# Performance work log

Measured on AMD Instinct MI355X. Metric: run time of the kernel, lower is better.

## Reference

```python
import jax, jax.numpy as jnp
import numpy as np

B, T, C = 4, 4096, 1024
HEAD = 128


def setup_inputs() -> dict:
    key = jax.random.key(0)
    k0, k1, k2, k3 = jax.random.split(key, 4)
    x = jax.random.normal(k0, (B, T, C), dtype=jnp.float32)
    # bias-free linear weights, stored as (in, out) so y = x @ W
    Wk = jax.random.normal(k1, (C, HEAD), dtype=jnp.float32) * (C ** -0.5)
    Wq = jax.random.normal(k2, (C, HEAD), dtype=jnp.float32) * (C ** -0.5)
    Wv = jax.random.normal(k3, (C, HEAD), dtype=jnp.float32) * (C ** -0.5)
    return {"x": x, "Wk": Wk, "Wq": Wq, "Wv": Wv}


def reference(x, Wk, Wq, Wv):
    Bx, Tx, Cx = x.shape
    k = x @ Wk            # [B,T,H]
    q = x @ Wq            # [B,T,H]
    v = x @ Wv            # [B,T,H]
    # NOTE: original code scales by C**-0.5 where C = n_embd (input dim), not head_size
    scale = Cx ** -0.5
    wei = jnp.einsum("bqh,bkh->bqk", q, k) * scale        # [B,T,T]
    causal = jnp.arange(Tx)[:, None] >= jnp.arange(Tx)[None, :]
    wei = jnp.where(causal, wei, -jnp.inf)
    wei = jax.nn.softmax(wei, axis=-1)
    # dropout rate is 0.0 in the source -> identity
    return jnp.einsum("bqk,bkh->bqh", wei, v)             # [B,T,H]
```

## Files before the change

### kernel.cpp

```cpp
#include <hip/hip_runtime.h>


typedef __bf16 bf16;
typedef bf16 bf16x8 __attribute__((ext_vector_type(8)));
typedef bf16 bf16x4 __attribute__((ext_vector_type(4)));
typedef float f32x4 __attribute__((ext_vector_type(4)));

#define L2E 1.4426950408889634f
#define TSEQ 4096
#define CDIM 1024
#define HDIM 128
#define MROWS 16384

#define GLDS(g, l)                                              \
  __builtin_amdgcn_global_load_lds(                             \
      (__attribute__((address_space(1))) void*)(g),             \
      (__attribute__((address_space(3))) void*)(l), 16, 0, 0)

static __device__ inline unsigned pkbf(float a, float b) {
  union { bf16 h; unsigned short u; } ua, ub;
  ua.h = (bf16)a; ub.h = (bf16)b;
  return ((unsigned)ub.u << 16) | (unsigned)ua.u;
}

__global__ __launch_bounds__(256) void wt_prep(const float* __restrict__ Wq,
                                               const float* __restrict__ Wk,
                                               const float* __restrict__ Wv,
                                               bf16* __restrict__ WT) {
  const int mode = blockIdx.y;
  const float* W = (mode == 0) ? Wq : (mode == 1) ? Wk : Wv;
  const int idx = blockIdx.x * 256 + threadIdx.x;
  const int n = idx >> 10;
  const int k = idx & 1023;
  WT[(size_t)mode * 131072 + idx] = (bf16)W[(size_t)k * HDIM + n];
}

__global__ __launch_bounds__(256) void qkv_gemm(const float* __restrict__ x,
                                                const bf16* __restrict__ WT,
                                                bf16* __restrict__ qb,
                                                bf16* __restrict__ kb,
                                                bf16* __restrict__ vT) {
  __shared__ __attribute__((aligned(16))) bf16 a_tile[128 * 32];
  __shared__ __attribute__((aligned(16))) bf16 b_tile[128 * 32];
  const int tid = threadIdx.x;
  const int wid = tid >> 6;
  const int lane = tid & 63;
  const int lr = lane & 15;
  const int lg = lane >> 4;
  const int wr = wid >> 1;
  const int wc = wid & 1;
  const int mode = blockIdx.y;
  const int m0 = blockIdx.x * 128;
  const bf16* wt = WT + (size_t)mode * 131072;

  int rowA[2], col8[2];
#pragma unroll
  for (int g = 0; g < 2; ++g) {
    const int idx8 = g * 256 + tid;
    rowA[g] = idx8 >> 2;
    col8[g] = (idx8 & 3) * 8;
  }

  f32x4 acc[4][4] = {};

  float4 fA[2][2];
  bf16x8 fB[2];
#pragma unroll
  for (int g = 0; g < 2; ++g) {
    const float* src = x + (size_t)(m0 + rowA[g]) * CDIM + col8[g];
    fA[g][0] = *(const float4*)src;
    fA[g][1] = *(const float4*)(src + 4);
    fB[g] = *(const bf16x8*)(wt + (size_t)rowA[g] * CDIM + col8[g]);
  }

#pragma unroll 1
  for (int kt = 0; kt < 32; ++kt) {
    __syncthreads();
#pragma unroll
    for (int g = 0; g < 2; ++g) {
      bf16x8 av;
      av[0] = (bf16)fA[g][0].x; av[1] = (bf16)fA[g][0].y;
      av[2] = (bf16)fA[g][0].z; av[3] = (bf16)fA[g][0].w;
      av[4] = (bf16)fA[g][1].x; av[5] = (bf16)fA[g][1].y;
      av[6] = (bf16)fA[g][1].z; av[7] = (bf16)fA[g][1].w;
      *(bf16x8*)&a_tile[rowA[g] * 32 + col8[g]] = av;
      *(bf16x8*)&b_tile[rowA[g] * 32 + col8[g]] = fB[g];
    }
    __syncthreads();
    if (kt + 1 < 32) {
#pragma unroll
      for (int g = 0; g < 2; ++g) {
        const float* src = x + (size_t)(m0 + rowA[g]) * CDIM + (kt + 1) * 32 + col8[g];
        fA[g][0] = *(const float4*)src;
        fA[g][1] = *(const float4*)(src + 4);
        fB[g] = *(const bf16x8*)(wt + (size_t)rowA[g] * CDIM + (kt + 1) * 32 + col8[g]);
      }
    }
    bf16x8 af[4], bfr[4];
#pragma unroll
    for (int r = 0; r < 4; ++r)
      af[r] = *(const bf16x8*)&a_tile[(wr * 64 + r * 16 + lr) * 32 + lg * 8];
#pragma unroll
    for (int c = 0; c < 4; ++c)
      bfr[c] = *(const bf16x8*)&b_tile[(wc * 64 + c * 16 + lr) * 32 + lg * 8];
#pragma unroll
    for (int r = 0; r < 4; ++r)
#pragma unroll
      for (int c = 0; c < 4; ++c)
        acc[r][c] = __builtin_amdgcn_mfma_f32_16x16x32_bf16(af[r], bfr[c], acc[r][c], 0, 0, 0);
  }

  if (mode < 2) {
    bf16* dst = (mode == 0) ? qb : kb;
    const float sc = (mode == 0) ? 0.03125f : 1.0f;
#pragma unroll
    for (int r = 0; r < 4; ++r)
#pragma unroll
      for (int c = 0; c < 4; ++c)
#pragma unroll
        for (int j = 0; j < 4; ++j) {
          const int row = m0 + wr * 64 + r * 16 + lg * 4 + j;
          const int col = wc * 64 + c * 16 + lr;
          dst[(size_t)row * HDIM + col] = (bf16)(acc[r][c][j] * sc);
        }
  } else {
#pragma unroll
    for (int r = 0; r < 4; ++r)
#pragma unroll
      for (int c = 0; c < 4; ++c) {
        const int row0 = m0 + wr * 64 + r * 16 + lg * 4;
        const int col = wc * 64 + c * 16 + lr;
        bf16x4 pv;
        pv[0] = (bf16)acc[r][c][0]; pv[1] = (bf16)acc[r][c][1];
        pv[2] = (bf16)acc[r][c][2]; pv[3] = (bf16)acc[r][c][3];
        *(bf16x4*)(vT + (size_t)col * MROWS + row0) = pv;
      }
  }
}

__global__ __launch_bounds__(256, 2) void attn_part(const bf16* __restrict__ qg,
                                                    const bf16* __restrict__ kb,
                                                    const bf16* __restrict__ vT,
                                                    bf16* __restrict__ po,
                                                    float* __restrict__ pm,
                                                    float* __restrict__ pl,
                                                    int cshift, int maxc) {
  __shared__ __attribute__((aligned(16))) char kv_lds[2][32768];
  __shared__ __attribute__((aligned(16))) bf16 p_lds[4][32][64];
  const int tid = threadIdx.x;
  const int wid = tid >> 6;
  const int lane = tid & 63;
  const int lr = lane & 15;
  const int lg = lane >> 4;
  const int b = blockIdx.z;
  const int c = blockIdx.y;
  const int qbase = blockIdx.x * 128;
  const int kv0 = c << cshift;
  if (kv0 >= qbase + 128) return;
  const int kvend = min(kv0 + (1 << cshift), qbase + 128);
  const int nt = (kvend - kv0) >> 6;
  const int qr0w = qbase + wid * 32;
  const int grp0 = blockIdx.x * 8 + wid * 2;
  const size_t qrow = (size_t)b * TSEQ + qr0w;

  const int wbase = wid * 4096;
  int ksrc[4], vsrc[4];
#pragma unroll
  for (int i = 0; i < 4; ++i) {
    const int o = wbase + i * 1024 + lane * 16;
    const int rk = o >> 8;
    ksrc[i] = rk * 256 + ((o & 255) ^ ((rk & 7) << 4));
    const int rv = o >> 7;
    vsrc[i] = rv * (MROWS * 2) + ((o & 127) ^ ((rv & 7) << 4));
  }
  const char* kgb = (const char*)kb + (size_t)b * TSEQ * 256;
  const char* vgb = (const char*)vT + (size_t)b * TSEQ * 2;

  const int msk = (lr & 7) << 4;
  const int m30 = (lr & 3) << 4;
  const int m6 = (lr & 4) << 4;
  const int lgx = (lg * 16) ^ m30;
  const int kreadA = lr * 256 + lgx + m6;
  const int kreadB = lr * 256 + lgx + (64 ^ m6);
  const int vreadA = 16384 + lr * 128 + lgx + m6;
  const int vreadB = 16384 + lr * 128 + lgx + (64 ^ m6);

  bf16x8 qa[4], qc[4];
#pragma unroll
  for (int d = 0; d < 4; ++d) {
    qa[d] = *(const bf16x8*)(qg + (qrow + lr) * HDIM + d * 32 + lg * 8);
    qc[d] = *(const bf16x8*)(qg + (qrow + 16 + lr) * HDIM + d * 32 + lg * 8);
  }

  f32x4 o0_[8] = {}, o1_[8] = {};
  float m0_ = -1e30f, l0_ = 0.0f;
  float m1_ = -1e30f, l1_ = 0.0f;

  {
    const char* ks = kgb + (size_t)kv0 * 256;
    const char* vs = vgb + (size_t)kv0 * 2;
#pragma unroll
    for (int i = 0; i < 4; ++i) {
      GLDS(ks + ksrc[i], &kv_lds[0][wbase + i * 1024]);
      GLDS(vs + vsrc[i], &kv_lds[0][16384 + wbase + i * 1024]);
    }
  }
  __syncthreads();

  int cur = 0;
  for (int t = 0; t < nt; ++t) {
    const int kvt = kv0 + (t << 6);
    if (t + 1 < nt) {
      const char* ks = kgb + (size_t)(kvt + 64) * 256;
      const char* vs = vgb + (size_t)(kvt + 64) * 2;
#pragma unroll
      for (int i = 0; i < 4; ++i) {
        GLDS(ks + ksrc[i], &kv_lds[cur ^ 1][wbase + i * 1024]);
        GLDS(vs + vsrc[i], &kv_lds[cur ^ 1][16384 + wbase + i * 1024]);
      }
    }
    if (kvt < qr0w + 32) {
      const char* kbuf = kv_lds[cur];
      f32x4 s0[4] = {}, s1[4] = {};
      __builtin_amdgcn_s_setprio(1);
#pragma unroll
      for (int nf = 0; nf < 4; ++nf) {
        const char* kb0 = kbuf + nf * 4096;
        bf16x8 kf;
        kf = *(const bf16x8*)(kb0 + kreadA);
        s0[nf] = __builtin_amdgcn_mfma_f32_16x16x32_bf16(kf, qa[0], s0[nf], 0, 0, 0);
        s1[nf] = __builtin_amdgcn_mfma_f32_16x16x32_bf16(kf, qc[0], s1[nf], 0, 0, 0);
        kf = *(const bf16x8*)(kb0 + kreadB);
        s0[nf] = __builtin_amdgcn_mfma_f32_16x16x32_bf16(kf, qa[1], s0[nf], 0, 0, 0);
        s1[nf] = __builtin_amdgcn_mfma_f32_16x16x32_bf16(kf, qc[1], s1[nf], 0, 0, 0);
        kf = *(const bf16x8*)(kb0 + kreadA + 128);
        s0[nf] = __builtin_amdgcn_mfma_f32_16x16x32_bf16(kf, qa[2], s0[nf], 0, 0, 0);
        s1[nf] = __builtin_amdgcn_mfma_f32_16x16x32_bf16(kf, qc[2], s1[nf], 0, 0, 0);
        kf = *(const bf16x8*)(kb0 + kreadB + 128);
        s0[nf] = __builtin_amdgcn_mfma_f32_16x16x32_bf16(kf, qa[3], s0[nf], 0, 0, 0);
        s1[nf] = __builtin_amdgcn_mfma_f32_16x16x32_bf16(kf, qc[3], s1[nf], 0, 0, 0);
      }
      __builtin_amdgcn_s_setprio(0);
      if (kvt + 63 >= qr0w) {
        const int q0 = qr0w + lr;
        const int q1 = q0 + 16;
#pragma unroll
        for (int nf = 0; nf < 4; ++nf)
#pragma unroll
          for (int j = 0; j < 4; ++j) {
            const int key = kvt + nf * 16 + lg * 4 + j;
            if (key > q0) s0[nf][j] = -1e30f;
            if (key > q1) s1[nf][j] = -1e30f;
          }
      }
      float r0 = fmaxf(fmaxf(s0[0][0], s0[0][1]), fmaxf(s0[0][2], s0[0][3]));
      float r1 = fmaxf(fmaxf(s1[0][0], s1[0][1]), fmaxf(s1[0][2], s1[0][3]));
#pragma unroll
      for (int nf = 1; nf < 4; ++nf) {
        r0 = fmaxf(r0, fmaxf(fmaxf(s0[nf][0], s0[nf][1]), fmaxf(s0[nf][2], s0[nf][3])));
        r1 = fmaxf(r1, fmaxf(fmaxf(s1[nf][0], s1[nf][1]), fmaxf(s1[nf][2], s1[nf][3])));
      }
      r0 = fmaxf(r0, __shfl_xor(r0, 16)); r0 = fmaxf(r0, __shfl_xor(r0, 32));
      r1 = fmaxf(r1, __shfl_xor(r1, 16)); r1 = fmaxf(r1, __shfl_xor(r1, 32));
      if (!__all(r0 <= m0_ + 8.0f && r1 <= m1_ + 8.0f)) {
        const float mn0 = fmaxf(m0_, r0), mn1 = fmaxf(m1_, r1);
        const float al0 = exp2f((m0_ - mn0) * L2E);
        const float al1 = exp2f((m1_ - mn1) * L2E);
        m0_ = mn0; m1_ = mn1;
        l0_ *= al0; l1_ *= al1;
#pragma unroll
        for (int o = 0; o < 8; ++o)
#pragma unroll
          for (int j = 0; j < 4; ++j) { o0_[o][j] *= al0; o1_[o][j] *= al1; }
      }
      float rs0 = 0.0f, rs1 = 0.0f;
#pragma unroll
      for (int nf = 0; nf < 4; ++nf)
#pragma unroll
        for (int j = 0; j < 4; ++j) {
          s0[nf][j] = exp2f((s0[nf][j] - m0_) * L2E); rs0 += s0[nf][j];
          s1[nf][j] = exp2f((s1[nf][j] - m1_) * L2E); rs1 += s1[nf][j];
        }
      {
        char* pw = (char*)p_lds + wid * 4096 + lr * 128;
#pragma unroll
        for (int nf = 0; nf < 4; ++nf) {
          uint2 w2;
          w2.x = pkbf(s0[nf][0], s0[nf][1]); w2.y = pkbf(s0[nf][2], s0[nf][3]);
          *(uint2*)(pw + (((nf * 32) + lg * 8) ^ msk)) = w2;
          w2.x = pkbf(s1[nf][0], s1[nf][1]); w2.y = pkbf(s1[nf][2], s1[nf][3]);
          *(uint2*)(pw + 2048 + (((nf * 32) + lg * 8) ^ msk)) = w2;
        }
      }
      rs0 += __shfl_xor(rs0, 16); rs0 += __shfl_xor(rs0, 32); l0_ += rs0;
      rs1 += __shfl_xor(rs1, 16); rs1 += __shfl_xor(rs1, 32); l1_ += rs1;
      asm volatile("s_waitcnt lgkmcnt(0)" ::: "memory");
      __builtin_amdgcn_sched_barrier(0);
      const char* pr = (const char*)p_lds + wid * 4096 + lr * 128;
      bf16x8 p00 = *(const bf16x8*)(pr + lgx + m6);
      bf16x8 p01 = *(const bf16x8*)(pr + lgx + (64 ^ m6));
      bf16x8 p10 = *(const bf16x8*)(pr + 2048 + lgx + m6);
      bf16x8 p11 = *(const bf16x8*)(pr + 2048 + lgx + (64 ^ m6));
      __builtin_amdgcn_s_setprio(1);
#pragma unroll
      for (int o = 0; o < 8; ++o) {
        bf16x8 vf;
        vf = *(const bf16x8*)(kbuf + vreadA + o * 2048);
        o0_[o] = __builtin_amdgcn_mfma_f32_16x16x32_bf16(vf, p00, o0_[o], 0, 0, 0);
        o1_[o] = __builtin_amdgcn_mfma_f32_16x16x32_bf16(vf, p10, o1_[o], 0, 0, 0);
        vf = *(const bf16x8*)(kbuf + vreadB + o * 2048);
        o0_[o] = __builtin_amdgcn_mfma_f32_16x16x32_bf16(vf, p01, o0_[o], 0, 0, 0);
        o1_[o] = __builtin_amdgcn_mfma_f32_16x16x32_bf16(vf, p11, o1_[o], 0, 0, 0);
      }
      __builtin_amdgcn_s_setprio(0);
    }
    __syncthreads();
    cur ^= 1;
  }

  const size_t slot0 = (size_t)(b * 256 + grp0) * maxc + c;
  const size_t slot1 = slot0 + maxc;
  bf16* pob0 = po + slot0 * (16 * HDIM);
  bf16* pob1 = po + slot1 * (16 * HDIM);
#pragma unroll
  for (int o = 0; o < 8; ++o) {
    bf16x4 pv;
    pv[0] = (bf16)o0_[o][0]; pv[1] = (bf16)o0_[o][1];
    pv[2] = (bf16)o0_[o][2]; pv[3] = (bf16)o0_[o][3];
    *(bf16x4*)(pob0 + lr * HDIM + o * 16 + lg * 4) = pv;
    pv[0] = (bf16)o1_[o][0]; pv[1] = (bf16)o1_[o][1];
    pv[2] = (bf16)o1_[o][2]; pv[3] = (bf16)o1_[o][3];
    *(bf16x4*)(pob1 + lr * HDIM + o * 16 + lg * 4) = pv;
  }
  if (lg == 0) {
    pm[slot0 * 16 + lr] = m0_; pl[slot0 * 16 + lr] = l0_;
    pm[slot1 * 16 + lr] = m1_; pl[slot1 * 16 + lr] = l1_;
  }
}

__global__ __launch_bounds__(256) void attn_merge(const bf16* __restrict__ po,
                                                  const float* __restrict__ pm,
                                                  const float* __restrict__ pl,
                                                  float* __restrict__ out,
                                                  int cshift, int maxc) {
  const int bg = blockIdx.x;
  const int g = bg & 255;
  const int nch = ((g << 4) >> cshift) + 1;
  const int row = threadIdx.x >> 4;
  const int d8 = (threadIdx.x & 15) * 8;
  const size_t slot0 = (size_t)bg * maxc;

  float M = -1e30f;
  for (int c = 0; c < nch; ++c) M = fmaxf(M, pm[(slot0 + c) * 16 + row]);
  float L = 0.0f;
  float acc[8] = {};
  for (int c = 0; c < nch; ++c) {
    const float w = exp2f((pm[(slot0 + c) * 16 + row] - M) * L2E);
    L += w * pl[(slot0 + c) * 16 + row];
    const bf16x8 v = *(const bf16x8*)(po + (slot0 + c) * (16 * HDIM) + row * HDIM + d8);
#pragma unroll
    for (int i = 0; i < 8; ++i) acc[i] += w * (float)v[i];
  }
  const float inv = 1.0f / L;
  f32x4 r0, r1;
#pragma unroll
  for (int i = 0; i < 4; ++i) { r0[i] = acc[i] * inv; r1[i] = acc[i + 4] * inv; }
  float* dst = out + (size_t)bg * (16 * HDIM) + row * HDIM + d8;
  *(f32x4*)dst = r0;
  *(f32x4*)(dst + 4) = r1;
}

extern "C" void kernel_launch(void* const* d_in, const int* in_sizes, int n_in,
                              void* d_out, int out_size, void* d_ws, size_t ws_size,
                              hipStream_t stream) {
  const float* x  = (const float*)d_in[0];
  const float* Wk = (const float*)d_in[1];
  const float* Wq = (const float*)d_in[2];
  const float* Wv = (const float*)d_in[3];
  float* out = (float*)d_out;

  char* ws = (char*)d_ws;
  bf16* qb = (bf16*)(ws);
  bf16* kb = (bf16*)(ws + 4194304);
  bf16* vT = (bf16*)(ws + 8388608);
  bf16* WT = (bf16*)(ws + 12582912);
  const size_t pbase = 13369344;

  int cshift, maxc;
  if (ws_size >= pbase + 8ull * 1024 * 4224) { cshift = 9;  maxc = 8; }
  else if (ws_size >= pbase + 4ull * 1024 * 4224) { cshift = 10; maxc = 4; }
  else { cshift = 12; maxc = 1; }
  bf16* po = (bf16*)(ws + pbase);
  float* pm = (float*)(ws + pbase + (size_t)maxc * 1024 * 16 * 128 * 2);
  float* pl = pm + (size_t)maxc * 1024 * 16;

  wt_prep<<<dim3(512, 3), 256, 0, stream>>>(Wq, Wk, Wv, WT);
  qkv_gemm<<<dim3(128, 3), 256, 0, stream>>>(x, WT, qb, kb, vT);
  attn_part<<<dim3(32, maxc, 4), 256, 0, stream>>>(qb, kb, vT, po, pm, pl, cshift, maxc);
  attn_merge<<<1024, 256, 0, stream>>>(po, pm, pl, out, cshift, maxc);
}
```

Before: 101.5 us.

## Tile V transpose into 64-row blocks, remap blocks across XCDs, defer row-sum shuffles

The projection kernel now stores V transposed in 64-key tiles, so each attention tile load reads one contiguous 16KB chunk instead of strided rows of length MROWS. When maxc is 8 the attention grid is remapped so that each XCD gets a balanced mix of causal chunk indices and shares K/V in its L2. The row-max shuffles now run only when the rescale branch is taken, and the row-sum shuffles are moved out of the loop and done once at the end. The lazy per-lane max depends on the wave-wide __all check still bounding the exponentials, which makes correctness of the rescale threshold harder to reason about.

Result: faster. 91.21 us (-10.1%).

```diff
diff --git a/kernel.cpp b/kernel.cpp
--- a/kernel.cpp
+++ b/kernel.cpp
@@ -133,7 +133,7 @@
         bf16x4 pv;
         pv[0] = (bf16)acc[r][c][0]; pv[1] = (bf16)acc[r][c][1];
         pv[2] = (bf16)acc[r][c][2]; pv[3] = (bf16)acc[r][c][3];
-        *(bf16x4*)(vT + (size_t)col * MROWS + row0) = pv;
+        *(bf16x4*)(vT + (size_t)(row0 >> 6) * 8192 + col * 64 + (row0 & 63)) = pv;
       }
   }
 }
@@ -152,15 +152,25 @@
   const int lane = tid & 63;
   const int lr = lane & 15;
   const int lg = lane >> 4;
-  const int b = blockIdx.z;
-  const int c = blockIdx.y;
-  const int qbase = blockIdx.x * 128;
+
+  int bx = blockIdx.x, c = blockIdx.y, b = blockIdx.z;
+  if (maxc == 8) {
+    const int p = blockIdx.x + 32 * (blockIdx.y + 8 * blockIdx.z);
+    const int xcd = p & 7;
+    const int s = p >> 3;
+    const int combo = s >> 5;
+    bx = s & 31;
+    b = combo;
+    c = (combo < 2) ? xcd : 7 - xcd;
+  }
+
+  const int qbase = bx * 128;
   const int kv0 = c << cshift;
   if (kv0 >= qbase + 128) return;
   const int kvend = min(kv0 + (1 << cshift), qbase + 128);
   const int nt = (kvend - kv0) >> 6;
   const int qr0w = qbase + wid * 32;
-  const int grp0 = blockIdx.x * 8 + wid * 2;
+  const int grp0 = bx * 8 + wid * 2;
   const size_t qrow = (size_t)b * TSEQ + qr0w;
 
   const int wbase = wid * 4096;
@@ -171,10 +181,10 @@
     const int rk = o >> 8;
     ksrc[i] = rk * 256 + ((o & 255) ^ ((rk & 7) << 4));
     const int rv = o >> 7;
-    vsrc[i] = rv * (MROWS * 2) + ((o & 127) ^ ((rv & 7) << 4));
+    vsrc[i] = rv * 128 + ((o & 127) ^ ((rv & 7) << 4));
   }
   const char* kgb = (const char*)kb + (size_t)b * TSEQ * 256;
-  const char* vgb = (const char*)vT + (size_t)b * TSEQ * 2;
+  const char* vgb = (const char*)vT + (size_t)b * TSEQ * 256;
 
   const int msk = (lr & 7) << 4;
   const int m30 = (lr & 3) << 4;
@@ -198,7 +208,7 @@
 
   {
     const char* ks = kgb + (size_t)kv0 * 256;
-    const char* vs = vgb + (size_t)kv0 * 2;
+    const char* vs = vgb + (size_t)kv0 * 256;
 #pragma unroll
     for (int i = 0; i < 4; ++i) {
       GLDS(ks + ksrc[i], &kv_lds[0][wbase + i * 1024]);
@@ -212,7 +222,7 @@
     const int kvt = kv0 + (t << 6);
     if (t + 1 < nt) {
       const char* ks = kgb + (size_t)(kvt + 64) * 256;
-      const char* vs = vgb + (size_t)(kvt + 64) * 2;
+      const char* vs = vgb + (size_t)(kvt + 64) * 256;
 #pragma unroll
       for (int i = 0; i < 4; ++i) {
         GLDS(ks + ksrc[i], &kv_lds[cur ^ 1][wbase + i * 1024]);
@@ -253,16 +263,16 @@
             if (key > q1) s1[nf][j] = -1e30f;
           }
       }
-      float r0 = fmaxf(fmaxf(s0[0][0], s0[0][1]), fmaxf(s0[0][2], s0[0][3]));
-      float r1 = fmaxf(fmaxf(s1[0][0], s1[0][1]), fmaxf(s1[0][2], s1[0][3]));
+      float rl0 = fmaxf(fmaxf(s0[0][0], s0[0][1]), fmaxf(s0[0][2], s0[0][3]));
+      float rl1 = fmaxf(fmaxf(s1[0][0], s1[0][1]), fmaxf(s1[0][2], s1[0][3]));
 #pragma unroll
       for (int nf = 1; nf < 4; ++nf) {
-        r0 = fmaxf(r0, fmaxf(fmaxf(s0[nf][0], s0[nf][1]), fmaxf(s0[nf][2], s0[nf][3])));
-        r1 = fmaxf(r1, fmaxf(fmaxf(s1[nf][0], s1[nf][1]), fmaxf(s1[nf][2], s1[nf][3])));
-      }
-      r0 = fmaxf(r0, __shfl_xor(r0, 16)); r0 = fmaxf(r0, __shfl_xor(r0, 32));
-      r1 = fmaxf(r1, __shfl_xor(r1, 16)); r1 = fmaxf(r1, __shfl_xor(r1, 32));
-      if (!__all(r0 <= m0_ + 8.0f && r1 <= m1_ + 8.0f)) {
+        rl0 = fmaxf(rl0, fmaxf(fmaxf(s0[nf][0], s0[nf][1]), fmaxf(s0[nf][2], s0[nf][3])));
+        rl1 = fmaxf(rl1, fmaxf(fmaxf(s1[nf][0], s1[nf][1]), fmaxf(s1[nf][2], s1[nf][3])));
+      }
+      if (!__all(rl0 <= m0_ + 8.0f && rl1 <= m1_ + 8.0f)) {
+        float r0 = fmaxf(rl0, __shfl_xor(rl0, 16)); r0 = fmaxf(r0, __shfl_xor(r0, 32));
+        float r1 = fmaxf(rl1, __shfl_xor(rl1, 16)); r1 = fmaxf(r1, __shfl_xor(r1, 32));
         const float mn0 = fmaxf(m0_, r0), mn1 = fmaxf(m1_, r1);
         const float al0 = exp2f((m0_ - mn0) * L2E);
         const float al1 = exp2f((m1_ - mn1) * L2E);
@@ -281,6 +291,7 @@
           s0[nf][j] = exp2f((s0[nf][j] - m0_) * L2E); rs0 += s0[nf][j];
           s1[nf][j] = exp2f((s1[nf][j] - m1_) * L2E); rs1 += s1[nf][j];
         }
+      l0_ += rs0; l1_ += rs1;
       {
         char* pw = (char*)p_lds + wid * 4096 + lr * 128;
 #pragma unroll
@@ -292,8 +303,6 @@
           *(uint2*)(pw + 2048 + (((nf * 32) + lg * 8) ^ msk)) = w2;
         }
       }
-      rs0 += __shfl_xor(rs0, 16); rs0 += __shfl_xor(rs0, 32); l0_ += rs0;
-      rs1 += __shfl_xor(rs1, 16); rs1 += __shfl_xor(rs1, 32); l1_ += rs1;
       asm volatile("s_waitcnt lgkmcnt(0)" ::: "memory");
       __builtin_amdgcn_sched_barrier(0);
       const char* pr = (const char*)p_lds + wid * 4096 + lr * 128;
@@ -317,6 +326,9 @@
     __syncthreads();
     cur ^= 1;
   }
+
+  l0_ += __shfl_xor(l0_, 16); l0_ += __shfl_xor(l0_, 32);
+  l1_ += __shfl_xor(l1_, 16); l1_ += __shfl_xor(l1_, 32);
 
   const size_t slot0 = (size_t)(b * 256 + grp0) * maxc + c;
   const size_t slot1 = slot0 + maxc;
```
